# Optimization experiments

Measured on AMD Instinct MI355X. Metric: run time of the kernel, lower is better.

Reference implementation:

```python
import jax, jax.numpy as jnp
import numpy as np

B, N, D, H = 16, 2048, 256, 256  # batch, sensor points, branch dim, hidden dim


def setup_inputs() -> dict:
    key = jax.random.key(0)
    ks = jax.random.split(key, 12)
    s = 0.02
    return {
        "x": jax.random.normal(ks[0], (B, N), dtype=jnp.float32),
        "grid": jax.random.uniform(ks[1], (N, 1), dtype=jnp.float32),  # cellcenters_nx
        "W1a": jax.random.normal(ks[2], (2, H), dtype=jnp.float32) * s,
        "b1a": jnp.zeros((H,), dtype=jnp.float32),
        "W1b": jax.random.normal(ks[3], (H, D), dtype=jnp.float32) * s,
        "b1b": jnp.zeros((D,), dtype=jnp.float32),
        "Wqkv": jax.random.normal(ks[4], (D, 3 * D), dtype=jnp.float32) * s,
        "W2a": jax.random.normal(ks[5], (D, H), dtype=jnp.float32) * s,
        "b2a": jnp.zeros((H,), dtype=jnp.float32),
        "W2b": jax.random.normal(ks[6], (H, D), dtype=jnp.float32) * s,
        "b2b": jnp.zeros((D,), dtype=jnp.float32),
    }


def reference(x, grid, W1a, b1a, W1b, b1b, Wqkv, W2a, b2a, W2b, b2b):
    b, n = x.shape
    # x.unsqueeze(-1) concat grid -> [B, N, 2]
    g = jnp.broadcast_to(grid[None, :, :], (b, n, 1))
    h = jnp.concatenate([x[..., None], g], axis=-1)
    # littleFNN Linear1: Linear -> GELU(exact) -> Linear
    h = jax.nn.gelu(h @ W1a + b1a, approximate=False) @ W1b + b1b  # [B, N, D]
    # SelfAttention: single fused qkv projection, no bias
    qkv = h @ Wqkv  # [B, N, 3D]
    q, k, v = jnp.split(qkv, 3, axis=-1)
    scale = jnp.asarray(qkv.shape[-1] // 3, h.dtype) ** -0.5
    scores = jnp.einsum("bid,bjd->bij", q, k) * scale  # [B, N, N]
    attn = jax.nn.softmax(scores, axis=-1)
    o = jnp.einsum("bij,bjd->bid", attn, v)  # [B, N, D]
    # littleFNN Linear2
    o = jax.nn.gelu(o @ W2a + b2a, approximate=False) @ W2b + b2b  # [B, N, D]
    return jnp.mean(o, axis=1)  # [B, D]
```

## Files before the change

### kernel.cpp

```cpp
#include <hip/hip_runtime.h>
#include <hip/hip_bf16.h>
#include <cmath>

typedef __attribute__((ext_vector_type(8))) short short8;
typedef __attribute__((ext_vector_type(4))) float f32x4;

#define MFMA16(a, b, c) __builtin_amdgcn_mfma_f32_16x16x32_bf16((a), (b), (c), 0, 0, 0)

static constexpr int BB = 16, NN = 2048, DD = 256, HH = 256;

__device__ inline unsigned short f2bf(float f) {
    union { float f; unsigned int u; } v; v.f = f;
    unsigned int r = v.u + 0x7fffu + ((v.u >> 16) & 1u);
    return (unsigned short)(r >> 16);
}
__device__ inline float bf2f(unsigned short u) {
    union { unsigned int u; float f; } v; v.u = ((unsigned int)u) << 16;
    return v.f;
}
__device__ inline float gelu_exact(float x) {
    return 0.5f * x * (1.0f + erff(x * 0.7071067811865475f));
}
__device__ inline void gload_lds16(const void* g, void* l) {
    __builtin_amdgcn_global_load_lds(
        (const __attribute__((address_space(1))) unsigned int*)g,
        (__attribute__((address_space(3))) unsigned int*)l, 16, 0, 0);
}
__device__ inline void fence_mem() { asm volatile("" ::: "memory"); }

__global__ __launch_bounds__(256) void transposeT_k(const float* __restrict__ W1b,
                                                    const float* __restrict__ Wqkv,
                                                    const float* __restrict__ W2a,
                                                    unsigned short* __restrict__ W1bT,
                                                    unsigned short* __restrict__ WqkvT,
                                                    unsigned short* __restrict__ W2aT) {
    __shared__ float tl[64][65];
    int bid = blockIdx.x;
    const float* src;
    unsigned short* dst;
    int N, tn, tk;
    if (bid < 16) {
        src = W1b; dst = W1bT; N = 256; tn = bid & 3; tk = bid >> 2;
    } else if (bid < 64) {
        int t2 = bid - 16;
        src = Wqkv; dst = WqkvT; N = 768; tn = t2 % 12; tk = t2 / 12;
    } else {
        int t2 = bid - 64;
        src = W2a; dst = W2aT; N = 256; tn = t2 & 3; tk = t2 >> 2;
    }
    int n0 = tn * 64, k0 = tk * 64;
    int t = threadIdx.x;
#pragma unroll
    for (int j = 0; j < 4; j++) {
        int row = (t >> 4) * 4 + j;
        f32x4 v = *(const f32x4*)(src + (size_t)(k0 + row) * N + n0 + (t & 15) * 4);
#pragma unroll
        for (int e = 0; e < 4; e++) tl[row][(t & 15) * 4 + e] = v[e];
    }
    __syncthreads();
    int n = t >> 2, cb = (t & 3) * 16;
    short8 a, b;
#pragma unroll
    for (int e = 0; e < 8; e++) {
        a[e] = (short)f2bf(tl[cb + e][n]);
        b[e] = (short)f2bf(tl[cb + 8 + e][n]);
    }
    *(short8*)(dst + (size_t)(n0 + n) * 256 + k0 + cb) = a;
    *(short8*)(dst + (size_t)(n0 + n) * 256 + k0 + cb + 8) = b;
}

__global__ __launch_bounds__(512) void ffn_qkv_k(const float* __restrict__ x,
                                                 const float* __restrict__ grd,
                                                 const float* __restrict__ W1a,
                                                 const float* __restrict__ b1a,
                                                 const unsigned short* __restrict__ W1bT,
                                                 const float* __restrict__ b1b,
                                                 const unsigned short* __restrict__ WqkvT,
                                                 unsigned short* __restrict__ qo,
                                                 unsigned short* __restrict__ ko,
                                                 unsigned short* __restrict__ vo) {
    __shared__ __attribute__((aligned(16))) char bstage[2][32768];
    __shared__ unsigned short h_lds[4][16 * 256];
    const int w = threadIdx.x >> 6, lane = threadIdx.x & 63;
    const int c = lane & 15, g = lane >> 4;
    const int qsub = w >> 1, nh = w & 1;
    const int rb = blockIdx.x * 64 + qsub * 16;
    const int bb = (blockIdx.x * 64) >> 11;
    const int rowinb = (rb & (NN - 1)) + c;

    const int p0r = rb + c;
    const float xv = x[p0r];
    const float gv = grd[p0r & (NN - 1)];
    short8 tf[8];
#pragma unroll
    for (int kc = 0; kc < 8; kc++) {
        int j0 = kc * 32 + g * 8;
#pragma unroll
        for (int e = 0; e < 8; e += 4) {
            f32x4 wa = *(const f32x4*)(W1a + j0 + e);
            f32x4 wb = *(const f32x4*)(W1a + 256 + j0 + e);
            f32x4 ba = *(const f32x4*)(b1a + j0 + e);
#pragma unroll
            for (int q = 0; q < 4; q++) {
                float v = xv * wa[q] + gv * wb[q] + ba[q];
                tf[kc][e + q] = (short)f2bf(gelu_exact(v));
            }
        }
    }

    const char* Bb0 = (const char*)W1bT;
    const char* Bb1 = (const char*)WqkvT;
    const char* Bb2 = (const char*)WqkvT + 256 * 512;
    const char* Bb3 = (const char*)WqkvT + 512 * 512;

#define STAGE_B(buf_, Bb_, kcp_) do {                                                    \
        _Pragma("unroll")                                                                \
        for (int i_ = 0; i_ < 4; i_++) {                                                 \
            int d_ = i_ * 8192 + w * 1024 + lane * 16;                                   \
            int row_ = d_ >> 7, sl_ = (d_ >> 4) & 7;                                     \
            gload_lds16(Bb_ + (size_t)row_ * 512 + (kcp_) * 128 +                        \
                            ((sl_ ^ (row_ & 7)) << 4),                                   \
                        &bstage[buf_][0] + d_);                                          \
        }                                                                                \
    } while (0)

    short8 hf[8];
#pragma unroll
    for (int kc = 0; kc < 8; kc++) hf[kc] = tf[kc];

    STAGE_B(0, Bb0, 0);

#pragma unroll
    for (int p = 0; p < 4; p++) {
        f32x4 acc[8];
#pragma unroll
        for (int n = 0; n < 8; n++) acc[n] = (f32x4){0.f, 0.f, 0.f, 0.f};

#pragma unroll
        for (int kcp = 0; kcp < 4; kcp++) {
            const int gi = p * 4 + kcp;
            if (gi + 1 < 16) {
                const int ni = gi + 1;
                const char* nb = (ni >> 2) == 0 ? Bb0 : (ni >> 2) == 1 ? Bb1
                                : (ni >> 2) == 2 ? Bb2 : Bb3;
                STAGE_B(ni & 1, nb, ni & 3);
                asm volatile("s_waitcnt vmcnt(4)" ::: "memory");
            } else {
                asm volatile("s_waitcnt vmcnt(0)" ::: "memory");
            }
            __builtin_amdgcn_s_barrier();
            fence_mem();

            const char* bl = &bstage[gi & 1][0];
#pragma unroll
            for (int sub = 0; sub < 2; sub++) {
                short8 a = (p == 0) ? tf[kcp * 2 + sub] : hf[kcp * 2 + sub];
#pragma unroll
                for (int n = 0; n < 8; n++) {
                    int addr = (nh * 128 + n * 16 + c) * 128 +
                               ((((sub << 2) | g) ^ (c & 7)) << 4);
                    short8 bfr = *(const short8*)(bl + addr);
                    if (p == 3) acc[n] = MFMA16(bfr, a, acc[n]);
                    else        acc[n] = MFMA16(a, bfr, acc[n]);
                }
            }
            fence_mem();
            __builtin_amdgcn_s_barrier();
            fence_mem();
        }

        if (p == 0) {
            unsigned short* hl = &h_lds[qsub][0];
#pragma unroll
            for (int n = 0; n < 8; n++) {
                int col = nh * 128 + n * 16 + c;
                float bv = b1b[col];
#pragma unroll
                for (int r = 0; r < 4; r++) {
                    int row = g * 4 + r;
                    hl[row * 256 + (col ^ ((row & 7) << 3))] = f2bf(acc[n][r] + bv);
                }
            }
            __syncthreads();
#pragma unroll
            for (int kc = 0; kc < 8; kc++) {
                hf[kc] = *(const short8*)(hl + c * 256 + ((kc * 32 + g * 8) ^ ((c & 7) << 3)));
            }
        } else if (p == 1) {
#pragma unroll
            for (int n = 0; n < 8; n++)
#pragma unroll
                for (int r = 0; r < 4; r++)
                    qo[(size_t)(rb + g * 4 + r) * 256 + nh * 128 + n * 16 + c] =
                        f2bf(acc[n][r] * 0.0625f);
        } else if (p == 2) {
#pragma unroll
            for (int n = 0; n < 8; n++)
#pragma unroll
                for (int r = 0; r < 4; r++)
                    ko[(size_t)(rb + g * 4 + r) * 256 + nh * 128 + n * 16 + c] =
                        f2bf(acc[n][r]);
        } else {
#pragma unroll
            for (int m = 0; m < 8; m++) {
#pragma unroll
                for (int r = 0; r < 4; r++) {
                    int dcol = nh * 128 + m * 16 + g * 4 + r;
                    vo[((size_t)(bb * 256 + dcol)) * NN + rowinb] = f2bf(acc[m][r]);
                }
            }
        }
    }
#undef STAGE_B
}

__global__ __launch_bounds__(512) void attn_k(const unsigned short* __restrict__ qb,
                                              const unsigned short* __restrict__ kb,
                                              const unsigned short* __restrict__ vTb,
                                              const unsigned short* __restrict__ W2aT,
                                              const float* __restrict__ b2a,
                                              float* __restrict__ bar) {
    __shared__ __attribute__((aligned(16))) char smem[64 * 512 + 256 * 128 + 8192 + 1024];
    char* klds = smem;
    char* vlds = smem + 32768;
    unsigned int* p_lds = (unsigned int*)(smem + 65536);
    float* exm = (float*)(smem + 65536 + 8192);
    float* exl = exm + 128;
    const int tid = threadIdx.x;
    const int w = tid >> 6, lane = tid & 63;
    const int c = lane & 15, g = lane >> 4;
    const int qsub = w & 3, dhalf = w >> 2;
    const int khalf = dhalf;
    const int bid = blockIdx.x;
    const int swz = (bid & 7) * 64 + (bid >> 3);
    const int b = swz >> 5;
    const int qt = swz & 31;
    const int qbase = qt * 64 + qsub * 16;
    constexpr int NT = NN / 64;

    const int sl_sub = lane >> 5;
    const int sl_col = (lane & 31) * 16;
    const int vl_row = lane >> 3;
    const size_t vl_off = (size_t)vl_row * (NN * 2) + (size_t)(((lane & 7) ^ vl_row) << 4);

    const short8* qp = (const short8*)(qb + (size_t)(b * NN + qbase + c) * DD + g * 8);
    short8 qf[8];
#pragma unroll
    for (int kc = 0; kc < 8; kc++) qf[kc] = qp[kc * 4];

    const char* kb_bytes = (const char*)(kb + (size_t)(b * NN) * DD);
    const char* vb_bytes = (const char*)(vTb + (size_t)(b * DD) * NN);
    const int kswz = (c & 7) << 4;
    const int pcs = c & 7;

#define STAGE_KV(kt_) do {                                                               \
        const char* gk = kb_bytes + ((size_t)((kt_) * 64 + 8 * w)) * 512;                \
        _Pragma("unroll")                                                                \
        for (int s_ = 0; s_ < 4; s_++) {                                                 \
            int row_lo = 2 * s_ + sl_sub;                                                \
            gload_lds16(gk + (size_t)row_lo * 512 + (sl_col ^ (row_lo << 4)),            \
                        klds + (8 * w + 2 * s_) * 512);                                  \
        }                                                                                \
        const char* gv = vb_bytes + (size_t)(32 * w) * (NN * 2) + (size_t)(kt_) * 128 + vl_off; \
        _Pragma("unroll")                                                                \
        for (int s_ = 0; s_ < 4; s_++) {                                                 \
            gload_lds16(gv + (size_t)(8 * s_) * (NN * 2),                                \
                        vlds + (32 * w + 8 * s_) * 128);                                 \
        }                                                                                \
    } while (0)

    f32x4 oacc[8];
#pragma unroll
    for (int i = 0; i < 8; i++) oacc[i] = (f32x4){0.f, 0.f, 0.f, 0.f};
    float mrun = -INFINITY;
    float lrun = 0.f;
    unsigned int* plw = p_lds + qsub * 512 + c * 32;

    for (int kt = 0; kt < NT; kt++) {
        STAGE_KV(kt);
        asm volatile("s_waitcnt vmcnt(0)" ::: "memory");
        __builtin_amdgcn_s_barrier();
        fence_mem();

        const char* klb = klds + (size_t)(khalf * 32) * 512;
        f32x4 s0 = (f32x4){0.f, 0.f, 0.f, 0.f};
        f32x4 s1 = (f32x4){0.f, 0.f, 0.f, 0.f};
        __builtin_amdgcn_s_setprio(1);
#pragma unroll
        for (int kc = 0; kc < 8; kc++) {
            short8 qv = qf[kc];
            int col = (kc * 64 + g * 16) ^ kswz;
            short8 kf0 = *(const short8*)(klb + (size_t)c * 512 + col);
            short8 kf1 = *(const short8*)(klb + (size_t)(c + 16) * 512 + col);
            s0 = MFMA16(kf0, qv, s0);
            s1 = MFMA16(kf1, qv, s1);
        }
        __builtin_amdgcn_s_setprio(0);

        float t0 = fmaxf(fmaxf(s0[0], s0[1]), fmaxf(s0[2], s0[3]));
        float t1 = fmaxf(fmaxf(s1[0], s1[1]), fmaxf(s1[2], s1[3]));
        float tmo = fmaxf(t0, t1);
        tmo = fmaxf(tmo, __shfl_xor(tmo, 16));
        tmo = fmaxf(tmo, __shfl_xor(tmo, 32));
        if (g == 0) exm[w * 16 + c] = tmo;
        fence_mem();
        __builtin_amdgcn_s_barrier();
        fence_mem();
        float tmax = fmaxf(tmo, exm[(w ^ 4) * 16 + c]);

        bool need = tmax > mrun + 8.f;
        if (__any(need)) {
            float mn = fmaxf(mrun, tmax);
            float corr = __expf(mrun - mn);
#pragma unroll
            for (int r = 0; r < 4; r++) s0[r] = __expf(s0[r] - mn);
#pragma unroll
            for (int r = 0; r < 4; r++) s1[r] = __expf(s1[r] - mn);
            lrun = lrun * corr + ((s0[0] + s0[1]) + (s0[2] + s0[3])) +
                   ((s1[0] + s1[1]) + (s1[2] + s1[3]));
            mrun = mn;
#pragma unroll
            for (int r = 0; r < 4; r++) {
                float cr = __shfl(corr, 20 * g + r);
#pragma unroll
                for (int nc = 0; nc < 8; nc++) oacc[nc][r] *= cr;
            }
        } else {
#pragma unroll
            for (int r = 0; r < 4; r++) s0[r] = __expf(s0[r] - mrun);
#pragma unroll
            for (int r = 0; r < 4; r++) s1[r] = __expf(s1[r] - mrun);
            lrun += ((s0[0] + s0[1]) + (s0[2] + s0[3])) +
                    ((s1[0] + s1[1]) + (s1[2] + s1[3]));
        }

        {
            int jb0 = khalf * 16 + 2 * g;
            int jb1 = khalf * 16 + 8 + 2 * g;
            unsigned int pw;
#pragma unroll
            for (int h = 0; h < 2; h++) {
                int j = jb0 + h;
                pw = (unsigned int)f2bf(s0[2 * h]) | ((unsigned int)f2bf(s0[2 * h + 1]) << 16);
                plw[(((j >> 2) ^ pcs) << 2) | (j & 3)] = pw;
                j = jb1 + h;
                pw = (unsigned int)f2bf(s1[2 * h]) | ((unsigned int)f2bf(s1[2 * h + 1]) << 16);
                plw[(((j >> 2) ^ pcs) << 2) | (j & 3)] = pw;
            }
        }
        fence_mem();
        __builtin_amdgcn_s_barrier();
        fence_mem();

        short8 pf0 = *(const short8*)(plw + ((g ^ pcs) << 2));
        short8 pf1 = *(const short8*)(plw + (((4 + g) ^ pcs) << 2));
        __builtin_amdgcn_s_setprio(1);
#pragma unroll
        for (int nc = 0; nc < 8; nc++) {
            const char* vr = vlds + (size_t)(dhalf * 128 + nc * 16 + c) * 128;
            short8 vf0 = *(const short8*)(vr + ((g ^ pcs) << 4));
            short8 vf1 = *(const short8*)(vr + (((4 + g) ^ pcs) << 4));
            oacc[nc] = MFMA16(pf0, vf0, oacc[nc]);
            oacc[nc] = MFMA16(pf1, vf1, oacc[nc]);
        }
        __builtin_amdgcn_s_setprio(0);

        fence_mem();
        __builtin_amdgcn_s_barrier();
        fence_mem();
    }
#undef STAGE_KV

    float lt = lrun;
    lt += __shfl_xor(lt, 16);
    lt += __shfl_xor(lt, 32);
    if (g == 0) exl[w * 16 + c] = lt;
    fence_mem();
    __builtin_amdgcn_s_barrier();
    fence_mem();
    lt += exl[(w ^ 4) * 16 + c];
    float inv_r[4];
#pragma unroll
    for (int r = 0; r < 4; r++) inv_r[r] = 1.f / __shfl(lt, 20 * g + r);

    unsigned short* ol = (unsigned short*)smem;
#pragma unroll
    for (int r = 0; r < 4; r++) {
        int row = 4 * g + r;
        int swr = (row & 7) << 3;
#pragma unroll
        for (int nc = 0; nc < 8; nc++) {
            int col = dhalf * 128 + nc * 16 + c;
            ol[qsub * 4096 + row * 256 + (col ^ swr)] = f2bf(oacc[nc][r] * inv_r[r]);
        }
    }
    fence_mem();
    __builtin_amdgcn_s_barrier();
    fence_mem();

    {
        const int wcol = w * 32;
        float colsum[2] = {0.f, 0.f};
#pragma unroll
        for (int q2 = 0; q2 < 4; q2++) {
            f32x4 acc2[2];
            acc2[0] = (f32x4){0.f, 0.f, 0.f, 0.f};
            acc2[1] = (f32x4){0.f, 0.f, 0.f, 0.f};
            const unsigned short* oq = ol + q2 * 4096;
            const int swc = (c & 7) << 3;
#pragma unroll
            for (int kc = 0; kc < 8; kc++) {
                short8 a = *(const short8*)(oq + c * 256 + ((kc * 32 + g * 8) ^ swc));
#pragma unroll
                for (int nc = 0; nc < 2; nc++) {
                    short8 bfr = *(const short8*)(W2aT + (size_t)(wcol + nc * 16 + c) * 256 + kc * 32 + g * 8);
                    acc2[nc] = MFMA16(a, bfr, acc2[nc]);
                }
            }
#pragma unroll
            for (int nc = 0; nc < 2; nc++) {
                float bv = b2a[wcol + nc * 16 + c];
                float s = 0.f;
#pragma unroll
                for (int r = 0; r < 4; r++) s += gelu_exact(acc2[nc][r] + bv);
                colsum[nc] += s;
            }
        }
#pragma unroll
        for (int nc = 0; nc < 2; nc++) {
            float s = colsum[nc];
            s += __shfl_xor(s, 16);
            s += __shfl_xor(s, 32);
            if (g == 0) atomicAdd(&bar[b * 256 + wcol + nc * 16 + c], s);
        }
    }
}

__global__ void final_k(const float* __restrict__ bar, const float* __restrict__ W2b,
                        const float* __restrict__ b2b, float* __restrict__ out) {
    int b = blockIdx.x, d = threadIdx.x;
    float s = 0.f;
    for (int h = 0; h < HH; h++) s += bar[b * HH + h] * W2b[h * DD + d];
    out[b * DD + d] = b2b[d] + s * (1.f / (float)NN);
}

extern "C" void kernel_launch(void* const* d_in, const int* in_sizes, int n_in,
                              void* d_out, int out_size, void* d_ws, size_t ws_size,
                              hipStream_t stream) {
    (void)in_sizes; (void)n_in; (void)out_size; (void)ws_size;
    const float* x    = (const float*)d_in[0];
    const float* grd  = (const float*)d_in[1];
    const float* W1a  = (const float*)d_in[2];
    const float* b1a  = (const float*)d_in[3];
    const float* W1b  = (const float*)d_in[4];
    const float* b1b  = (const float*)d_in[5];
    const float* Wqkv = (const float*)d_in[6];
    const float* W2a  = (const float*)d_in[7];
    const float* b2a  = (const float*)d_in[8];
    const float* W2b  = (const float*)d_in[9];
    const float* b2b  = (const float*)d_in[10];
    float* out = (float*)d_out;

    char* ws = (char*)d_ws;
    const size_t MB = 1024 * 1024;
    unsigned short* q_buf  = (unsigned short*)(ws + 0);
    unsigned short* k_buf  = (unsigned short*)(ws + 16 * MB);
    unsigned short* vT_buf = (unsigned short*)(ws + 32 * MB);
    unsigned short* W1bT   = (unsigned short*)(ws + 80 * MB);
    unsigned short* WqkvT  = (unsigned short*)(ws + 80 * MB + 512 * 1024);
    unsigned short* W2aT   = (unsigned short*)(ws + 81 * MB);
    float*          bar    = (float*)(ws + 81 * MB + 256 * 1024);

    transposeT_k<<<dim3(80), 256, 0, stream>>>(W1b, Wqkv, W2a, W1bT, WqkvT, W2aT);
    ffn_qkv_k<<<dim3(512), 512, 0, stream>>>(x, grd, W1a, b1a, W1bT, b1b, WqkvT,
                                             q_buf, k_buf, vT_buf);
    hipMemsetAsync(bar, 0, BB * HH * sizeof(float), stream);
    attn_k<<<dim3(512), 512, 0, stream>>>(q_buf, k_buf, vT_buf, W2aT, b2a, bar);
    final_k<<<dim3(BB), 256, 0, stream>>>(bar, W2b, b2b, out);
}
```

Baseline: 239.4 us.

## Compute full key tile per wave to drop cross-wave softmax barriers

Each wave now computes QK^T scores for all 64 keys of the tile, instead of splitting keys between wave pairs that share a query block. Row max, row sum and the bf16 P tile therefore stay within one wave. This removes the exm/exl LDS exchange, the barrier per tile for the max reduction, the barrier between the P write and the P read, and the final row-sum barrier. The price is that the QK^T MFMA work and K LDS reads are duplicated across the two waves that share a query block. Each wave also gets its own private P buffer.

```diff
diff --git a/kernel.cpp b/kernel.cpp
--- a/kernel.cpp
+++ b/kernel.cpp
@@ -220,17 +220,14 @@
                                               const unsigned short* __restrict__ W2aT,
                                               const float* __restrict__ b2a,
                                               float* __restrict__ bar) {
-    __shared__ __attribute__((aligned(16))) char smem[64 * 512 + 256 * 128 + 8192 + 1024];
+    __shared__ __attribute__((aligned(16))) char smem[81920];
     char* klds = smem;
     char* vlds = smem + 32768;
     unsigned int* p_lds = (unsigned int*)(smem + 65536);
-    float* exm = (float*)(smem + 65536 + 8192);
-    float* exl = exm + 128;
     const int tid = threadIdx.x;
     const int w = tid >> 6, lane = tid & 63;
     const int c = lane & 15, g = lane >> 4;
     const int qsub = w & 3, dhalf = w >> 2;
-    const int khalf = dhalf;
     const int bid = blockIdx.x;
     const int swz = (bid & 7) * 64 + (bid >> 3);
     const int b = swz >> 5;
@@ -251,6 +248,7 @@
     const char* kb_bytes = (const char*)(kb + (size_t)(b * NN) * DD);
     const char* vb_bytes = (const char*)(vTb + (size_t)(b * DD) * NN);
     const int kswz = (c & 7) << 4;
+    const int pswz = (c & 7) << 2;
     const int pcs = c & 7;
 
 #define STAGE_KV(kt_) do {                                                               \
@@ -274,7 +272,7 @@
     for (int i = 0; i < 8; i++) oacc[i] = (f32x4){0.f, 0.f, 0.f, 0.f};
     float mrun = -INFINITY;
     float lrun = 0.f;
-    unsigned int* plw = p_lds + qsub * 512 + c * 32;
+    unsigned int* plw = p_lds + w * 512 + c * 32;
 
     for (int kt = 0; kt < NT; kt++) {
         STAGE_KV(kt);
@@ -282,42 +280,43 @@
         __builtin_amdgcn_s_barrier();
         fence_mem();
 
-        const char* klb = klds + (size_t)(khalf * 32) * 512;
-        f32x4 s0 = (f32x4){0.f, 0.f, 0.f, 0.f};
-        f32x4 s1 = (f32x4){0.f, 0.f, 0.f, 0.f};
+        f32x4 s[4];
+#pragma unroll
+        for (int t = 0; t < 4; t++) s[t] = (f32x4){0.f, 0.f, 0.f, 0.f};
         __builtin_amdgcn_s_setprio(1);
 #pragma unroll
         for (int kc = 0; kc < 8; kc++) {
             short8 qv = qf[kc];
             int col = (kc * 64 + g * 16) ^ kswz;
-            short8 kf0 = *(const short8*)(klb + (size_t)c * 512 + col);
-            short8 kf1 = *(const short8*)(klb + (size_t)(c + 16) * 512 + col);
-            s0 = MFMA16(kf0, qv, s0);
-            s1 = MFMA16(kf1, qv, s1);
+#pragma unroll
+            for (int t = 0; t < 4; t++) {
+                short8 kf = *(const short8*)(klds + (size_t)(16 * t + c) * 512 + col);
+                s[t] = MFMA16(kf, qv, s[t]);
+            }
         }
         __builtin_amdgcn_s_setprio(0);
 
-        float t0 = fmaxf(fmaxf(s0[0], s0[1]), fmaxf(s0[2], s0[3]));
-        float t1 = fmaxf(fmaxf(s1[0], s1[1]), fmaxf(s1[2], s1[3]));
-        float tmo = fmaxf(t0, t1);
-        tmo = fmaxf(tmo, __shfl_xor(tmo, 16));
-        tmo = fmaxf(tmo, __shfl_xor(tmo, 32));
-        if (g == 0) exm[w * 16 + c] = tmo;
-        fence_mem();
-        __builtin_amdgcn_s_barrier();
-        fence_mem();
-        float tmax = fmaxf(tmo, exm[(w ^ 4) * 16 + c]);
+        float tm[4];
+#pragma unroll
+        for (int t = 0; t < 4; t++)
+            tm[t] = fmaxf(fmaxf(s[t][0], s[t][1]), fmaxf(s[t][2], s[t][3]));
+        float tmax = fmaxf(fmaxf(tm[0], tm[1]), fmaxf(tm[2], tm[3]));
+        tmax = fmaxf(tmax, __shfl_xor(tmax, 16));
+        tmax = fmaxf(tmax, __shfl_xor(tmax, 32));
 
         bool need = tmax > mrun + 8.f;
         if (__any(need)) {
             float mn = fmaxf(mrun, tmax);
             float corr = __expf(mrun - mn);
 #pragma unroll
-            for (int r = 0; r < 4; r++) s0[r] = __expf(s0[r] - mn);
-#pragma unroll
-            for (int r = 0; r < 4; r++) s1[r] = __expf(s1[r] - mn);
-            lrun = lrun * corr + ((s0[0] + s0[1]) + (s0[2] + s0[3])) +
-                   ((s1[0] + s1[1]) + (s1[2] + s1[3]));
+            for (int t = 0; t < 4; t++)
+#pragma unroll
+                for (int r = 0; r < 4; r++) s[t][r] = __expf(s[t][r] - mn);
+            float a0 = (s[0][0] + s[0][1]) + (s[0][2] + s[0][3]);
+            float a1 = (s[1][0] + s[1][1]) + (s[1][2] + s[1][3]);
+            float a2 = (s[2][0] + s[2][1]) + (s[2][2] + s[2][3]);
+            float a3 = (s[3][0] + s[3][1]) + (s[3][2] + s[3][3]);
+            lrun = lrun * corr + ((a0 + a1) + (a2 + a3));
             mrun = mn;
 #pragma unroll
             for (int r = 0; r < 4; r++) {
@@ -327,33 +326,28 @@
             }
         } else {
 #pragma unroll
-            for (int r = 0; r < 4; r++) s0[r] = __expf(s0[r] - mrun);
-#pragma unroll
-            for (int r = 0; r < 4; r++) s1[r] = __expf(s1[r] - mrun);
-            lrun += ((s0[0] + s0[1]) + (s0[2] + s0[3])) +
-                    ((s1[0] + s1[1]) + (s1[2] + s1[3]));
-        }
-
-        {
-            int jb0 = khalf * 16 + 2 * g;
-            int jb1 = khalf * 16 + 8 + 2 * g;
-            unsigned int pw;
+            for (int t = 0; t < 4; t++)
+#pragma unroll
+                for (int r = 0; r < 4; r++) s[t][r] = __expf(s[t][r] - mrun);
+            float a0 = (s[0][0] + s[0][1]) + (s[0][2] + s[0][3]);
+            float a1 = (s[1][0] + s[1][1]) + (s[1][2] + s[1][3]);
+            float a2 = (s[2][0] + s[2][1]) + (s[2][2] + s[2][3]);
+            float a3 = (s[3][0] + s[3][1]) + (s[3][2] + s[3][3]);
+            lrun += (a0 + a1) + (a2 + a3);
+        }
+
+#pragma unroll
+        for (int t = 0; t < 4; t++) {
 #pragma unroll
             for (int h = 0; h < 2; h++) {
-                int j = jb0 + h;
-                pw = (unsigned int)f2bf(s0[2 * h]) | ((unsigned int)f2bf(s0[2 * h + 1]) << 16);
-                plw[(((j >> 2) ^ pcs) << 2) | (j & 3)] = pw;
-                j = jb1 + h;
-                pw = (unsigned int)f2bf(s1[2 * h]) | ((unsigned int)f2bf(s1[2 * h + 1]) << 16);
-                plw[(((j >> 2) ^ pcs) << 2) | (j & 3)] = pw;
-            }
-        }
-        fence_mem();
-        __builtin_amdgcn_s_barrier();
-        fence_mem();
-
-        short8 pf0 = *(const short8*)(plw + ((g ^ pcs) << 2));
-        short8 pf1 = *(const short8*)(plw + (((4 + g) ^ pcs) << 2));
+                unsigned int pw = (unsigned int)f2bf(s[t][2 * h]) |
+                                  ((unsigned int)f2bf(s[t][2 * h + 1]) << 16);
+                plw[(8 * t + 2 * g + h) ^ pswz] = pw;
+            }
+        }
+        short8 pf0 = *(const short8*)(plw + ((4 * g) ^ pswz));
+        short8 pf1 = *(const short8*)(plw + ((16 + 4 * g) ^ pswz));
+
         __builtin_amdgcn_s_setprio(1);
 #pragma unroll
         for (int nc = 0; nc < 8; nc++) {
@@ -374,11 +368,6 @@
     float lt = lrun;
     lt += __shfl_xor(lt, 16);
     lt += __shfl_xor(lt, 32);
-    if (g == 0) exl[w * 16 + c] = lt;
-    fence_mem();
-    __builtin_amdgcn_s_barrier();
-    fence_mem();
-    lt += exl[(w ^ 4) * 16 + c];
     float inv_r[4];
 #pragma unroll
     for (int r = 0; r < 4; r++) inv_r[r] = 1.f / __shfl(lt, 20 * g + r);
@@ -420,18 +409,18 @@
 #pragma unroll
             for (int nc = 0; nc < 2; nc++) {
                 float bv = b2a[wcol + nc * 16 + c];
-                float s = 0.f;
-#pragma unroll
-                for (int r = 0; r < 4; r++) s += gelu_exact(acc2[nc][r] + bv);
-                colsum[nc] += s;
+                float s2 = 0.f;
+#pragma unroll
+                for (int r = 0; r < 4; r++) s2 += gelu_exact(acc2[nc][r] + bv);
+                colsum[nc] += s2;
             }
         }
 #pragma unroll
         for (int nc = 0; nc < 2; nc++) {
-            float s = colsum[nc];
-            s += __shfl_xor(s, 16);
-            s += __shfl_xor(s, 32);
-            if (g == 0) atomicAdd(&bar[b * 256 + wcol + nc * 16 + c], s);
+            float s2 = colsum[nc];
+            s2 += __shfl_xor(s2, 16);
+            s2 += __shfl_xor(s2, 32);
+            if (g == 0) atomicAdd(&bar[b * 256 + wcol + nc * 16 + c], s2);
         }
     }
 }
```

After: 275.2 us. 1.15x slower.

## Split K/V staging to prefetch next K tile, use exp2 and packed bf16 convert

Applied to the files above, without the earlier changes.

K and V tile loads are split so that the next K tile is issued during the softmax of the current tile, and V is waited on separately with partial vmcnt waits. This overlaps global-to-LDS loads with compute instead of draining all loads at the top of every iteration. The Q scale also folds in log2(e) so softmax can use exp2f, and P is packed to bf16 with the v_cvt_pk_bf16_f32 instruction instead of manual rounding. The risks are races on the single K buffer if the waits or barriers are wrong, and slight rounding differences.

```diff
diff --git a/kernel.cpp b/kernel.cpp
--- a/kernel.cpp
+++ b/kernel.cpp
@@ -27,6 +27,11 @@
         (__attribute__((address_space(3))) unsigned int*)l, 16, 0, 0);
 }
 __device__ inline void fence_mem() { asm volatile("" ::: "memory"); }
+__device__ inline unsigned int cvtpk_bf16(float lo, float hi) {
+    unsigned int r;
+    asm("v_cvt_pk_bf16_f32 %0, %1, %2" : "=v"(r) : "v"(lo), "v"(hi));
+    return r;
+}
 
 __global__ __launch_bounds__(256) void transposeT_k(const float* __restrict__ W1b,
                                                     const float* __restrict__ Wqkv,
@@ -192,7 +197,7 @@
 #pragma unroll
                 for (int r = 0; r < 4; r++)
                     qo[(size_t)(rb + g * 4 + r) * 256 + nh * 128 + n * 16 + c] =
-                        f2bf(acc[n][r] * 0.0625f);
+                        f2bf(acc[n][r] * (0.0625f * 1.4426950408889634f));
         } else if (p == 2) {
 #pragma unroll
             for (int n = 0; n < 8; n++)
@@ -220,7 +225,7 @@
                                               const unsigned short* __restrict__ W2aT,
                                               const float* __restrict__ b2a,
                                               float* __restrict__ bar) {
-    __shared__ __attribute__((aligned(16))) char smem[64 * 512 + 256 * 128 + 8192 + 1024];
+    __shared__ __attribute__((aligned(16))) char smem[74752];
     char* klds = smem;
     char* vlds = smem + 32768;
     unsigned int* p_lds = (unsigned int*)(smem + 65536);
@@ -253,7 +258,7 @@
     const int kswz = (c & 7) << 4;
     const int pcs = c & 7;
 
-#define STAGE_KV(kt_) do {                                                               \
+#define STAGE_K(kt_) do {                                                                \
         const char* gk = kb_bytes + ((size_t)((kt_) * 64 + 8 * w)) * 512;                \
         _Pragma("unroll")                                                                \
         for (int s_ = 0; s_ < 4; s_++) {                                                 \
@@ -261,6 +266,8 @@
             gload_lds16(gk + (size_t)row_lo * 512 + (sl_col ^ (row_lo << 4)),            \
                         klds + (8 * w + 2 * s_) * 512);                                  \
         }                                                                                \
+    } while (0)
+#define STAGE_V(kt_) do {                                                                \
         const char* gv = vb_bytes + (size_t)(32 * w) * (NN * 2) + (size_t)(kt_) * 128 + vl_off; \
         _Pragma("unroll")                                                                \
         for (int s_ = 0; s_ < 4; s_++) {                                                 \
@@ -276,9 +283,11 @@
     float lrun = 0.f;
     unsigned int* plw = p_lds + qsub * 512 + c * 32;
 
+    STAGE_K(0);
+
     for (int kt = 0; kt < NT; kt++) {
-        STAGE_KV(kt);
-        asm volatile("s_waitcnt vmcnt(0)" ::: "memory");
+        STAGE_V(kt);
+        asm volatile("s_waitcnt vmcnt(4)" ::: "memory");
         __builtin_amdgcn_s_barrier();
         fence_mem();
 
@@ -308,14 +317,16 @@
         fence_mem();
         float tmax = fmaxf(tmo, exm[(w ^ 4) * 16 + c]);
 
+        if (kt + 1 < NT) STAGE_K(kt + 1);
+
         bool need = tmax > mrun + 8.f;
         if (__any(need)) {
             float mn = fmaxf(mrun, tmax);
-            float corr = __expf(mrun - mn);
-#pragma unroll
-            for (int r = 0; r < 4; r++) s0[r] = __expf(s0[r] - mn);
-#pragma unroll
-            for (int r = 0; r < 4; r++) s1[r] = __expf(s1[r] - mn);
+            float corr = exp2f(mrun - mn);
+#pragma unroll
+            for (int r = 0; r < 4; r++) s0[r] = exp2f(s0[r] - mn);
+#pragma unroll
+            for (int r = 0; r < 4; r++) s1[r] = exp2f(s1[r] - mn);
             lrun = lrun * corr + ((s0[0] + s0[1]) + (s0[2] + s0[3])) +
                    ((s1[0] + s1[1]) + (s1[2] + s1[3]));
             mrun = mn;
@@ -327,9 +338,9 @@
             }
         } else {
 #pragma unroll
-            for (int r = 0; r < 4; r++) s0[r] = __expf(s0[r] - mrun);
-#pragma unroll
-            for (int r = 0; r < 4; r++) s1[r] = __expf(s1[r] - mrun);
+            for (int r = 0; r < 4; r++) s0[r] = exp2f(s0[r] - mrun);
+#pragma unroll
+            for (int r = 0; r < 4; r++) s1[r] = exp2f(s1[r] - mrun);
             lrun += ((s0[0] + s0[1]) + (s0[2] + s0[3])) +
                     ((s1[0] + s1[1]) + (s1[2] + s1[3]));
         }
@@ -337,18 +348,20 @@
         {
             int jb0 = khalf * 16 + 2 * g;
             int jb1 = khalf * 16 + 8 + 2 * g;
-            unsigned int pw;
 #pragma unroll
             for (int h = 0; h < 2; h++) {
                 int j = jb0 + h;
-                pw = (unsigned int)f2bf(s0[2 * h]) | ((unsigned int)f2bf(s0[2 * h + 1]) << 16);
-                plw[(((j >> 2) ^ pcs) << 2) | (j & 3)] = pw;
+                plw[(((j >> 2) ^ pcs) << 2) | (j & 3)] = cvtpk_bf16(s0[2 * h], s0[2 * h + 1]);
                 j = jb1 + h;
-                pw = (unsigned int)f2bf(s1[2 * h]) | ((unsigned int)f2bf(s1[2 * h + 1]) << 16);
-                plw[(((j >> 2) ^ pcs) << 2) | (j & 3)] = pw;
-            }
-        }
-        fence_mem();
+                plw[(((j >> 2) ^ pcs) << 2) | (j & 3)] = cvtpk_bf16(s1[2 * h], s1[2 * h + 1]);
+            }
+        }
+        fence_mem();
+        if (kt + 1 < NT) {
+            asm volatile("s_waitcnt vmcnt(4)" ::: "memory");
+        } else {
+            asm volatile("s_waitcnt vmcnt(0)" ::: "memory");
+        }
         __builtin_amdgcn_s_barrier();
         fence_mem();
 
@@ -369,7 +382,8 @@
         __builtin_amdgcn_s_barrier();
         fence_mem();
     }
-#undef STAGE_KV
+#undef STAGE_K
+#undef STAGE_V
 
     float lt = lrun;
     lt += __shfl_xor(lt, 16);
@@ -420,18 +434,18 @@
 #pragma unroll
             for (int nc = 0; nc < 2; nc++) {
                 float bv = b2a[wcol + nc * 16 + c];
-                float s = 0.f;
-#pragma unroll
-                for (int r = 0; r < 4; r++) s += gelu_exact(acc2[nc][r] + bv);
-                colsum[nc] += s;
+                float s2 = 0.f;
+#pragma unroll
+                for (int r = 0; r < 4; r++) s2 += gelu_exact(acc2[nc][r] + bv);
+                colsum[nc] += s2;
             }
         }
 #pragma unroll
         for (int nc = 0; nc < 2; nc++) {
-            float s = colsum[nc];
-            s += __shfl_xor(s, 16);
-            s += __shfl_xor(s, 32);
-            if (g == 0) atomicAdd(&bar[b * 256 + wcol + nc * 16 + c], s);
+            float s2 = colsum[nc];
+            s2 += __shfl_xor(s2, 16);
+            s2 += __shfl_xor(s2, 32);
+            if (g == 0) atomicAdd(&bar[b * 256 + wcol + nc * 16 + c], s2);
         }
     }
 }
```

Measured after the change: 197.8 us. -17.4%, faster.
